# Optimization experiments

Hardware: AMD Instinct MI355X
Metric: run time of the kernel (lower is better)

## Reference

```python
import jax, jax.numpy as jnp
import numpy as np

B, L, H = 1024, 11, 128          # batch, seq_len-1 observations, cde_hidden_dim
VF, IF = 512, 256                # v_f_len, i_f_len
C = H + 1                        # control channels = time + reduced features
SUBSTEPS = 4                     # fixed RK4 substeps per eval interval (stand-in for solver step control)


def setup_inputs() -> dict:
    key = jax.random.key(0)
    ks = jax.random.split(key, 12)
    rn = lambda k, shape, s: jax.random.normal(k, shape, jnp.float32) * s
    F = VF + IF
    inp = {
        'fv': rn(ks[0], (B, L, VF), 1.0),
        'fi': rn(ks[1], (B, L, IF), 1.0),
        # strictly increasing timestamps
        'ts': jnp.cumsum(jax.random.uniform(ks[2], (B, L + 1), jnp.float32) * 0.1 + 0.01, axis=1),
        'w_red': rn(ks[3], (F, H), F ** -0.5), 'b_red': jnp.zeros((H,), jnp.float32),
        'w_init': rn(ks[4], (C, H), C ** -0.5), 'b_init': jnp.zeros((H,), jnp.float32),
        'w_h1': rn(ks[5], (H, H), H ** -0.5), 'b_h1': jnp.zeros((H,), jnp.float32),
        'w_h2': rn(ks[6], (H, H), H ** -0.5), 'b_h2': jnp.zeros((H,), jnp.float32),
        'w_out': rn(ks[7], (H, H * C), H ** -0.5), 'b_out': jnp.zeros((H * C,), jnp.float32),
        'w_r1': rn(ks[8], (H, 128), H ** -0.5), 'b_r1': jnp.zeros((128,), jnp.float32),
        'w_r2': rn(ks[9], (128, 6), 128 ** -0.5), 'b_r2': jnp.zeros((6,), jnp.float32),
    }
    return inp


def reference(fv, fi, ts, w_red, b_red, w_init, b_init, w_h1, b_h1, w_h2, b_h2,
              w_out, b_out, w_r1, b_r1, w_r2, b_r2):
    # fuse ('cat') + reduction_net
    fused = jnp.concatenate([fv, fi], axis=-1) @ w_red + b_red            # [B,L,H]
    tsd = (ts - ts[:, :1])[:, 1:, None]                                   # [B,L,1]
    x = jnp.concatenate([tsd, fused], axis=-1)                            # [B,L,C] control path; knots at t=0..L-1
    z0 = x[:, 0] @ w_init + b_init                                        # initial hidden state, [B,H]

    def field(z):                                                         # CDEFunc: [B,H] -> [B,H,C]
        h1 = jax.nn.relu(z @ w_h1 + b_h1)
        h2 = jax.nn.relu(h1 @ w_h2 + b_h2)
        return jnp.tanh(h2 @ w_out + b_out).reshape(-1, H, C)

    def dXdt(t):                                                          # piecewise-linear interpolation derivative
        idx = jnp.clip(jnp.floor(t).astype(jnp.int32), 0, L - 2)
        return x[:, idx + 1] - x[:, idx]                                  # [B,C]

    def vf(t, z):                                                         # dz/dt = f(z) @ dX/dt
        return jnp.einsum('bhc,bc->bh', field(z), dXdt(t))

    eval_times = jnp.linspace(0.1, 1.0, 10, dtype=jnp.float32)
    hstep = (eval_times[1] - eval_times[0]) / SUBSTEPS

    def rk4(z, t):
        k1 = vf(t, z)
        k2 = vf(t + hstep / 2, z + hstep / 2 * k1)
        k3 = vf(t + hstep / 2, z + hstep / 2 * k2)
        k4 = vf(t + hstep, z + hstep * k3)
        return z + hstep / 6 * (k1 + 2 * k2 + 2 * k3 + k4)

    def interval(z, t0):
        def body(zc, j):
            return rk4(zc, t0 + j * hstep), None
        z2, _ = jax.lax.scan(body, z, jnp.arange(SUBSTEPS, dtype=jnp.float32))
        return z2, z2

    _, zs = jax.lax.scan(interval, z0, eval_times[:-1])                   # [9,B,H]
    h_T = jnp.concatenate([z0[None], zs], axis=0).transpose(1, 0, 2)      # [B,10,H]

    a = h_T @ w_r1 + b_r1
    a = jnp.where(a > 0, a, 0.1 * a)                                      # LeakyReLU(0.1)
    poses = a @ w_r2 + b_r2                                               # [B,10,6]
    return poses, h_T[:, -1, :]
```

## Files before the change

kernel.cpp:

```cpp
#include <hip/hip_runtime.h>
#include <stdint.h>

typedef float   f32x4 __attribute__((ext_vector_type(4)));
typedef float   f32x2 __attribute__((ext_vector_type(2)));
typedef int     i32x4 __attribute__((ext_vector_type(4)));
typedef int     i32x2 __attribute__((ext_vector_type(2)));
typedef __bf16  bf16x8 __attribute__((ext_vector_type(8)));

#define DEV __device__ __forceinline__

DEV uint16_t f2bf(float f){
  uint32_t u = __float_as_uint(f);
  u += 0x7fffu + ((u >> 16) & 1u);
  return (uint16_t)(u >> 16);
}
DEV uint32_t pkbf(float lo, float hi){
  uint32_t r;
  asm("v_cvt_pk_bf16_f32 %0, %1, %2" : "=v"(r) : "v"(lo), "v"(hi));
  return r;
}
DEV uint32_t aoff(uint32_t row, uint32_t q){ return (row << 8) + (q ^ ((row & 7u) << 4)); }

DEV f32x4 MFMA(bf16x8 a, bf16x8 b, f32x4 c){
  return __builtin_amdgcn_mfma_f32_16x16x32_bf16(a, b, c, 0, 0, 0);
}
DEV bf16x8 as_bf(i32x4 v){ union { i32x4 i; bf16x8 b; } u; u.i = v; return u.b; }

DEV uint64_t ld_ic64(const void* p){
  return __hip_atomic_load((const uint64_t*)p, __ATOMIC_RELAXED, __HIP_MEMORY_SCOPE_AGENT);
}
DEV void st_ic64(void* p, uint64_t v){
  __hip_atomic_store((uint64_t*)p, v, __ATOMIC_RELAXED, __HIP_MEMORY_SCOPE_AGENT);
}

__global__ __launch_bounds__(256) void pose_convW(const float* __restrict__ src,
    uint16_t* __restrict__ Wg, uint16_t* __restrict__ w0f)
{
  __shared__ float tile[32][256];
  const float SC = 2.8853900817779268f;
  int bk = blockIdx.x & 3, bn = blockIdx.x >> 2;
  int k0 = bk * 32, n0 = bn * 256;
  int t = threadIdx.x;
  for (int r = 0; r < 32; r++){
    int n = n0 + t;
    tile[r][t] = (n < 16512) ? src[(size_t)(k0 + r) * 16512 + n] : 0.f;
  }
  __syncthreads();
  int n = n0 + t;
  if (n < 16512){
    int c = n % 129, hfull = n / 129;
    int ht = hfull >> 2;
    #pragma unroll
    for (int o = 0; o < 4; o++){
      uint32_t w0 = (uint32_t)f2bf(tile[o*8+0][t]*SC) | ((uint32_t)f2bf(tile[o*8+1][t]*SC) << 16);
      uint32_t w1 = (uint32_t)f2bf(tile[o*8+2][t]*SC) | ((uint32_t)f2bf(tile[o*8+3][t]*SC) << 16);
      uint32_t w2 = (uint32_t)f2bf(tile[o*8+4][t]*SC) | ((uint32_t)f2bf(tile[o*8+5][t]*SC) << 16);
      uint32_t w3 = (uint32_t)f2bf(tile[o*8+6][t]*SC) | ((uint32_t)f2bf(tile[o*8+7][t]*SC) << 16);
      i32x4 val = { (int)w0, (int)w1, (int)w2, (int)w3 };
      uint32_t kg = (uint32_t)(k0 + o*8);
      if (c > 0){
        uint32_t r = (uint32_t)(c - 1)*4 + (hfull & 3);
        uint32_t byte = (uint32_t)ht*131072u + r*256u + ((kg*2u) ^ ((r & 7u) << 4));
        *(i32x4*)((char*)Wg + byte) = val;
      } else {
        uint32_t r0 = (uint32_t)(hfull & 3);
        uint32_t byte = (uint32_t)ht*4096u + (kg >> 5)*1024u + (r0 + 16u*((kg >> 3) & 3u))*16u;
        *(i32x4*)((char*)w0f + byte) = val;
      }
    }
  }
}

__global__ __launch_bounds__(256) void pose_convC(const float* __restrict__ w_h1,
    const float* __restrict__ w_h2, uint32_t* __restrict__ w1f, uint32_t* __restrict__ w2f)
{
  const float* src = blockIdx.x ? w_h2 : w_h1;
  uint32_t* dst = blockIdx.x ? w2f : w1f;
  int t = threadIdx.x;
  for (int ii = 0; ii < 32; ii++){
    int u = t*32 + ii;
    int p = u & 3, l = (u >> 2) & 63, kb = (u >> 8) & 3, Mt = u >> 10;
    int k = kb*32 + (l >> 4)*8 + 2*p;
    int n = Mt*16 + (l & 15);
    uint32_t v = (uint32_t)f2bf(src[(size_t)k*128 + n]) |
                 ((uint32_t)f2bf(src[(size_t)(k+1)*128 + n]) << 16);
    dst[u] = v;
  }
}

__global__ __launch_bounds__(256) void pose_misc(const float* __restrict__ b_out,
    const float* __restrict__ ts, float* __restrict__ bo_f, float* __restrict__ bo_t,
    float* __restrict__ d0t)
{
  const float SC = 2.8853900817779268f;
  int i = blockIdx.x * 256 + threadIdx.x;
  if (i < 16512){
    int c = i % 129, h = i / 129;
    if (c == 0) bo_t[h] = b_out[i] * SC;
    else        bo_f[(size_t)(c-1)*128 + h] = b_out[i] * SC;
  }
  if (i < 1024) d0t[i] = ts[i*12 + 2] - ts[i*12 + 1];
}

__global__ __launch_bounds__(256) void pose_fused(
    const float* __restrict__ fv, const float* __restrict__ fi,
    const float* __restrict__ w_red, const float* __restrict__ b_red,
    float* __restrict__ F0, float* __restrict__ d0f)
{
  __shared__ float pk[128][16];
  __shared__ float res[16][128];
  const int b0 = blockIdx.x * 8;
  const int t = threadIdx.x;
  const int h = t & 127, sg = t >> 7;
  float acc[8] = {0.f,0.f,0.f,0.f,0.f,0.f,0.f,0.f};
  for (int p = 0; p < 6; p++){
    __syncthreads();
    { const int s  = t >> 4;
      const int ch = (t & 15) * 8;
      const int b  = b0 + (s & 7);
      const int ll = s >> 3;
      const int kb = p*128 + ch;
      const float* src = (kb < 512) ? (fv + ((size_t)b*11 + ll)*512 + kb)
                                    : (fi + ((size_t)b*11 + ll)*256 + (kb - 512));
      float v[8];
      #pragma unroll
      for (int j = 0; j < 8; j++) v[j] = src[j];
      #pragma unroll
      for (int j = 0; j < 8; j++) pk[ch + j][s] = v[j];
    }
    __syncthreads();
    #pragma unroll 4
    for (int kk = 0; kk < 128; kk++){
      const float wv = w_red[(size_t)(p*128 + kk)*128 + h];
      f32x4 v0 = *(const f32x4*)&pk[kk][sg*8];
      f32x4 v1 = *(const f32x4*)&pk[kk][sg*8 + 4];
      acc[0] += v0.x*wv; acc[1] += v0.y*wv; acc[2] += v0.z*wv; acc[3] += v0.w*wv;
      acc[4] += v1.x*wv; acc[5] += v1.y*wv; acc[6] += v1.z*wv; acc[7] += v1.w*wv;
    }
  }
  __syncthreads();
  const float br = b_red[h];
  #pragma unroll
  for (int si = 0; si < 8; si++) res[sg*8 + si][h] = acc[si] + br;
  __syncthreads();
  if (sg == 0){
    #pragma unroll
    for (int si = 0; si < 8; si++){
      const int b = b0 + si;
      const float f0 = res[si][h];
      const float f1 = res[8 + si][h];
      F0[(size_t)b*128 + h] = f0;
      d0f[(size_t)h*1024 + b] = f1 - f0;
    }
  }
}

DEV uint32_t zaddr(int b, int h){
  return (uint32_t)(b >> 7)*32768u + (uint32_t)((b >> 4) & 7)*4096u + (uint32_t)(h >> 5)*1024u
       + ((uint32_t)(b & 15) + 16u*(((uint32_t)h & 31u) >> 3))*16u + ((uint32_t)h & 7u)*2u;
}

__global__ __launch_bounds__(512) void pose_init(
    const float* __restrict__ F0, const float* __restrict__ ts,
    const float* __restrict__ w_init, const float* __restrict__ b_init,
    const float* __restrict__ d0f, const float* __restrict__ d0t,
    float* __restrict__ z_base, uint16_t* __restrict__ zfG,
    float* __restrict__ hT, float* __restrict__ S)
{
  __shared__ float Ft[128][64];
  const int b0 = blockIdx.x * 64;
  const int t = threadIdx.x;
  { const int b = t >> 3, ch = (t & 7)*16;
    #pragma unroll
    for (int j = 0; j < 16; j++) Ft[ch + j][b] = F0[(size_t)(b0 + b)*128 + ch + j];
  }
  __syncthreads();
  const int h = t & 127, rg = t >> 7;
  float acc[16];
  const float w0 = w_init[h], bi = b_init[h];
  #pragma unroll
  for (int r = 0; r < 16; r++){
    const int b = b0 + rg*16 + r;
    acc[r] = (ts[b*12 + 1] - ts[b*12 + 0]) * w0 + bi;
  }
  #pragma unroll 2
  for (int j = 0; j < 128; j++){
    const float wv = w_init[(j + 1)*128 + h];
    const float* pr = &Ft[j][rg*16];
    #pragma unroll
    for (int q = 0; q < 4; q++){
      f32x4 v = *(const f32x4*)(pr + q*4);
      acc[q*4+0] += v.x*wv; acc[q*4+1] += v.y*wv; acc[q*4+2] += v.z*wv; acc[q*4+3] += v.w*wv;
    }
  }
  #pragma unroll
  for (int r = 0; r < 16; r++){
    const int b = b0 + rg*16 + r;
    const float z = acc[r];
    z_base[(size_t)b*128 + h] = z;
    hT[(size_t)b*1280 + h] = z;
    *(uint16_t*)((char*)zfG + zaddr(b, h)) = f2bf(z);
  }
  if (t < 64){
    const int b = b0 + t;
    float s = d0t[b];
    for (int j = 0; j < 128; j++) s += d0f[(size_t)j*1024 + b];
    S[b] = s;
  }
}

__global__ __launch_bounds__(1024, 1)
__attribute__((amdgpu_num_vgpr(128)))
void pose_persist(
    const uint16_t* __restrict__ Wg, const uint32_t* __restrict__ w1f,
    const uint32_t* __restrict__ w2f, const uint16_t* __restrict__ w0f,
    const float* __restrict__ b1, const float* __restrict__ b2,
    const float* __restrict__ bo_f, const float* __restrict__ bo_t,
    const float* __restrict__ d0f, const float* __restrict__ d0t,
    const float* __restrict__ Sv, const float* __restrict__ z_base,
    uint16_t* __restrict__ zfG, float* __restrict__ hT, uint32_t* __restrict__ bar)
{
  __shared__ __align__(16) char Lds[163840];
  const uint32_t HB = 131072u;
  const int t    = threadIdx.x;
  const int blk  = blockIdx.x;
  const int bt   = blk & 7;
  const int ht   = blk >> 3;
  const int w    = t >> 6, l = t & 63;
  const int l15  = l & 15, l4g = l >> 4;
  const int m8   = w & 7;
  const int half = w >> 3;
  const int m4   = w & 3;
  const int nq   = w >> 2;

  { const i32x4* src = (const i32x4*)((const char*)Wg + (size_t)ht*131072);
    i32x4* dst = (i32x4*)Lds;
    #pragma unroll
    for (int i = 0; i < 8; i++) dst[t + 1024*i] = src[t + 1024*i];
  }

  const float* d0q  = d0f + (size_t)l4g*1024 + bt*128 + nq*32 + l15;
  const float* d0tq = d0t + bt*128 + nq*32 + l15;

  const int bl = t >> 2, hp = t & 3;
  const float HS = 0x1.999996p-6f;
  const float C2 = HS * 0.5f, C6 = HS / 6.f;
  float zb = 0.f, Sb = 0.f, av = 0.f;
  if (t < 512){
    zb = z_base[(size_t)(bt*128 + bl)*128 + ht*4 + hp];
    Sb = Sv[bt*128 + bl];
  }
  uint32_t* cnt = bar + bt*32;
  uint32_t* go  = bar + 256 + bt*32;
  const uint32_t zsl_off = (uint32_t)bt*32768u;
  __syncthreads();

  #pragma unroll 1
  for (int e = 0; e < 144; e++){
    { const char* zsrc = (const char*)zfG + (size_t)(e & 1)*262144 + zsl_off;
      #pragma unroll
      for (int i = 0; i < 2; i++){
        union { uint64_t q[2]; i32x4 v; } u;
        u.q[0] = ld_ic64(zsrc + t*16 + i*16384);
        u.q[1] = ld_ic64(zsrc + t*16 + i*16384 + 8);
        *(i32x4*)(Lds + HB + t*16 + i*16384) = u.v;
      }
    }
    __syncthreads();

    uint32_t pv1[4][2];
    { bf16x8 w1A[4];
      #pragma unroll
      for (int kb = 0; kb < 4; kb++)
        w1A[kb] = as_bf(*(const i32x4*)((const char*)w1f + (size_t)(m8*4 + kb)*1024 + l*16));
      const f32x4 b1v = *(const f32x4*)(b1 + m8*16 + l4g*4);
      #pragma unroll
      for (int nt2 = 0; nt2 < 4; nt2++){
        bf16x8 bz[4];
        #pragma unroll
        for (int kb = 0; kb < 4; kb++)
          bz[kb] = as_bf(*(const i32x4*)(Lds + HB + (uint32_t)(half*4 + nt2)*4096u + kb*1024 + l*16));
        f32x4 a = {0.f,0.f,0.f,0.f};
        #pragma unroll
        for (int kb = 0; kb < 4; kb++) a = MFMA(w1A[kb], bz[kb], a);
        pv1[nt2][0] = pkbf(fmaxf(a.x + b1v.x, 0.f), fmaxf(a.y + b1v.y, 0.f));
        pv1[nt2][1] = pkbf(fmaxf(a.z + b1v.z, 0.f), fmaxf(a.w + b1v.w, 0.f));
      }
    }
    __syncthreads();

    #pragma unroll
    for (int nt2 = 0; nt2 < 4; nt2++){
      const int col = half*64 + nt2*16 + l15;
      i32x2 pv = { (int)pv1[nt2][0], (int)pv1[nt2][1] };
      *(i32x2*)(Lds + HB + aoff((uint32_t)col, (uint32_t)(m8*16 + l4g*4)*2)) = pv;
    }
    __syncthreads();

    bf16x8 bh1[4];
    #pragma unroll
    for (int kb = 0; kb < 4; kb++)
      bh1[kb] = as_bf(*(const i32x4*)(Lds + HB + aoff((uint32_t)(m8*16 + l15), kb*64 + l4g*16)));
    __syncthreads();
    #pragma unroll
    for (int i = 0; i < 4; i++){
      const int Mt = half*4 + i;
      bf16x8 a2[4];
      #pragma unroll
      for (int kb = 0; kb < 4; kb++)
        a2[kb] = as_bf(*(const i32x4*)((const char*)w2f + (size_t)(Mt*4 + kb)*1024 + l*16));
      f32x4 acc = {0.f,0.f,0.f,0.f};
      #pragma unroll
      for (int kb = 0; kb < 4; kb++) acc = MFMA(a2[kb], bh1[kb], acc);
      const f32x4 b2v = *(const f32x4*)(b2 + Mt*16 + l4g*4);
      i32x2 pv = { (int)pkbf(fmaxf(acc.x + b2v.x, 0.f), fmaxf(acc.y + b2v.y, 0.f)),
                   (int)pkbf(fmaxf(acc.z + b2v.z, 0.f), fmaxf(acc.w + b2v.w, 0.f)) };
      *(i32x2*)(Lds + HB + aoff((uint32_t)(m8*16 + l15), (uint32_t)(Mt*16 + l4g*4)*2)) = pv;
    }
    __syncthreads();

    bf16x8 bh2[2][4];
    #pragma unroll
    for (int n2 = 0; n2 < 2; n2++)
      #pragma unroll
      for (int kb = 0; kb < 4; kb++)
        bh2[n2][kb] = as_bf(*(const i32x4*)(Lds + HB +
            aoff((uint32_t)(nq*32 + n2*16 + l15), kb*64 + l4g*16)));
    __syncthreads();

    f32x4 oacc[2];
    oacc[0] = (f32x4){0.f,0.f,0.f,0.f};
    oacc[1] = (f32x4){0.f,0.f,0.f,0.f};

    #pragma unroll 2
    for (int i = 0; i < 8; i++){
      const int Mt = m4*8 + i;
      bf16x8 A[4];
      #pragma unroll
      for (int kb = 0; kb < 4; kb++)
        A[kb] = as_bf(*(const i32x4*)(Lds + aoff((uint32_t)(Mt*16 + l15), kb*64 + l4g*16)));
      const f32x4 bo4 = *(const f32x4*)(bo_f + (size_t)(Mt*4 + l4g)*128 + ht*4);
      #pragma unroll
      for (int n2 = 0; n2 < 2; n2++){
        f32x4 acc = {0.f,0.f,0.f,0.f};
        #pragma unroll
        for (int kb = 0; kb < 4; kb++) acc = MFMA(A[kb], bh2[n2][kb], acc);
        f32x4 rr;
        rr.x = __builtin_amdgcn_rcpf(__builtin_amdgcn_exp2f(acc.x + bo4.x) + 1.f);
        rr.y = __builtin_amdgcn_rcpf(__builtin_amdgcn_exp2f(acc.y + bo4.y) + 1.f);
        rr.z = __builtin_amdgcn_rcpf(__builtin_amdgcn_exp2f(acc.z + bo4.z) + 1.f);
        rr.w = __builtin_amdgcn_rcpf(__builtin_amdgcn_exp2f(acc.w + bo4.w) + 1.f);
        oacc[n2] += rr * d0q[((size_t)Mt << 12) + n2*16];
      }
    }
    if (m4 == 0){
      bf16x8 A0[4];
      #pragma unroll
      for (int kb = 0; kb < 4; kb++)
        A0[kb] = as_bf(*(const i32x4*)((const char*)w0f + (size_t)ht*4096 + kb*1024 + l*16));
      const f32x4 bt4 = *(const f32x4*)(bo_t + ht*4);
      #pragma unroll
      for (int n2 = 0; n2 < 2; n2++){
        f32x4 acc = {0.f,0.f,0.f,0.f};
        #pragma unroll
        for (int kb = 0; kb < 4; kb++) acc = MFMA(A0[kb], bh2[n2][kb], acc);
        f32x4 rr;
        rr.x = __builtin_amdgcn_rcpf(__builtin_amdgcn_exp2f(acc.x + bt4.x) + 1.f);
        rr.y = __builtin_amdgcn_rcpf(__builtin_amdgcn_exp2f(acc.y + bt4.y) + 1.f);
        rr.z = __builtin_amdgcn_rcpf(__builtin_amdgcn_exp2f(acc.z + bt4.z) + 1.f);
        rr.w = __builtin_amdgcn_rcpf(__builtin_amdgcn_exp2f(acc.w + bt4.w) + 1.f);
        const float dc = (l4g == 0) ? d0tq[n2*16] : 0.f;
        oacc[n2] += rr * dc;
      }
    }

    #pragma unroll
    for (int n2 = 0; n2 < 2; n2++){
      #pragma unroll
      for (int c = 0; c < 4; c++){
        float v = oacc[n2][c];
        v += __shfl_xor(v, 16, 64);
        v += __shfl_xor(v, 32, 64);
        oacc[n2][c] = v;
      }
    }
    if (l < 16){
      #pragma unroll
      for (int n2 = 0; n2 < 2; n2++){
        const int b = nq*32 + n2*16 + l15;
        *(f32x4*)(Lds + HB + m4*2048 + b*16) = oacc[n2];
      }
    }
    __syncthreads();

    if (t < 512){
      float psum = 0.f;
      #pragma unroll
      for (int m = 0; m < 4; m++)
        psum += *(const float*)(Lds + HB + m*2048 + bl*16 + hp*4);
      const float kk = Sb - 2.f*psum;
      const int st = e & 3;
      float ze;
      if (st == 0){      av = kk;        ze = zb + C2*kk; }
      else if (st == 1){ av += 2.f*kk;   ze = zb + C2*kk; }
      else if (st == 2){ av += 2.f*kk;   ze = zb + HS*kk; }
      else {
        zb += C6*(av + kk); ze = zb;
        if ((e & 15) == 15)
          hT[(size_t)(bt*128 + bl)*1280 + (size_t)((e >> 4) + 1)*128 + ht*4 + hp] = zb;
      }
      if (e < 143){
        const uint32_t a0 = pkbf(ze, __shfl_xor(ze, 1, 64));
        const uint32_t b0 = (uint32_t)__shfl_xor((int)a0, 2, 64);
        if ((t & 3) == 0){
          uint64_t zw = (uint64_t)a0 | ((uint64_t)b0 << 32);
          char* zdst = (char*)zfG + (size_t)((e + 1) & 1)*262144 + zsl_off
                     + (bl >> 4)*4096 + (ht >> 3)*1024
                     + ((bl & 15) + 16*((ht >> 1) & 3))*16 + (ht & 1)*8;
          st_ic64(zdst, zw);
        }
        asm volatile("s_waitcnt vmcnt(0)" ::: "memory");
        if ((t & 63) == 0){
          uint32_t a = __hip_atomic_fetch_add(cnt, 1u, __ATOMIC_RELAXED, __HIP_MEMORY_SCOPE_AGENT);
          if (a == 256u*(uint32_t)(e + 1) - 1u)
            __hip_atomic_store(go, (uint32_t)(e + 1), __ATOMIC_RELAXED, __HIP_MEMORY_SCOPE_AGENT);
        }
      }
    }

    if (e < 143){
      const uint32_t ep = (uint32_t)(e + 1);
      int spins = 0;
      while (__hip_atomic_load(go, __ATOMIC_RELAXED, __HIP_MEMORY_SCOPE_AGENT) < ep){
        __builtin_amdgcn_s_sleep(2);
        if (++spins > (1 << 20)) break;
      }
      asm volatile("" ::: "memory");
    }
  }
}

__global__ __launch_bounds__(256) void pose_readout(
    const float* __restrict__ hT, const float* __restrict__ w_r1, const float* __restrict__ b_r1,
    const float* __restrict__ w_r2, const float* __restrict__ b_r2,
    float* __restrict__ out_poses, float* __restrict__ out_z)
{
  if (blockIdx.x >= 320){
    const int cb = blockIdx.x - 320;
    const int base = cb*2048 + threadIdx.x*4;
    #pragma unroll
    for (int p = 0; p < 2; p++){
      const int i = base + p*1024;
      const int b = i >> 7, h = i & 127;
      *(f32x4*)(out_z + i) = *(const f32x4*)(hT + (size_t)b*1280 + 1152 + h);
    }
    return;
  }
  __shared__ float htl[128][32];
  __shared__ float al[32][128];
  const int r0 = blockIdx.x * 32;
  const int t = threadIdx.x;
  { const int row = t >> 3, ch = (t & 7)*16;
    #pragma unroll
    for (int j = 0; j < 16; j++)
      htl[ch + j][row] = hT[(size_t)(r0 + row)*128 + ch + j];
  }
  __syncthreads();
  const int j = t & 127, rg = t >> 7;
  float a[16];
  const float bj = b_r1[j];
  #pragma unroll
  for (int r = 0; r < 16; r++) a[r] = bj;
  #pragma unroll 2
  for (int kk = 0; kk < 128; kk++){
    const float wv = w_r1[(size_t)kk*128 + j];
    const float* pr = &htl[kk][rg*16];
    #pragma unroll
    for (int q = 0; q < 4; q++){
      f32x4 v = *(const f32x4*)(pr + q*4);
      a[q*4+0] += v.x*wv; a[q*4+1] += v.y*wv; a[q*4+2] += v.z*wv; a[q*4+3] += v.w*wv;
    }
  }
  #pragma unroll
  for (int r = 0; r < 16; r++){
    float v = a[r];
    al[rg*16 + r][j] = (v > 0.f) ? v : 0.1f*v;
  }
  __syncthreads();
  if (t < 192){
    const int row = t / 6, p = t % 6;
    float s = b_r2[p];
    const float* ar = al[row];
    #pragma unroll 4
    for (int jj = 0; jj < 128; jj++) s += ar[jj] * w_r2[jj*6 + p];
    out_poses[(size_t)(r0 + row)*6 + p] = s;
  }
}

extern "C" void kernel_launch(void* const* d_in, const int* in_sizes, int n_in,
                              void* d_out, int out_size, void* d_ws, size_t ws_size,
                              hipStream_t stream)
{
  (void)in_sizes; (void)n_in; (void)out_size; (void)ws_size;
  const float* fv    = (const float*)d_in[0];
  const float* fi    = (const float*)d_in[1];
  const float* ts    = (const float*)d_in[2];
  const float* w_red = (const float*)d_in[3];
  const float* b_red = (const float*)d_in[4];
  const float* w_init= (const float*)d_in[5];
  const float* b_init= (const float*)d_in[6];
  const float* w_h1  = (const float*)d_in[7];
  const float* b_h1  = (const float*)d_in[8];
  const float* w_h2  = (const float*)d_in[9];
  const float* b_h2  = (const float*)d_in[10];
  const float* w_out = (const float*)d_in[11];
  const float* b_out = (const float*)d_in[12];
  const float* w_r1  = (const float*)d_in[13];
  const float* b_r1  = (const float*)d_in[14];
  const float* w_r2  = (const float*)d_in[15];
  const float* b_r2  = (const float*)d_in[16];

  char* p = (char*)d_ws;
  auto take = [&](size_t n){ char* r = p; p += (n + 255) & ~(size_t)255; return r; };
  uint32_t* bar   = (uint32_t*)take(4096);
  uint16_t* Wg    = (uint16_t*)take((size_t)32*131072);
  uint16_t* w0f   = (uint16_t*)take((size_t)32*4096);
  uint32_t* w1f   = (uint32_t*)take(32768);
  uint32_t* w2f   = (uint32_t*)take(32768);
  float* bo_f     = (float*)take((size_t)128*128*4);
  float* bo_t     = (float*)take(128*4);
  float* d0f      = (float*)take((size_t)128*1024*4);
  float* d0t      = (float*)take(1024*4);
  float* Sv       = (float*)take(1024*4);
  float* F0       = (float*)take((size_t)1024*128*4);
  float* z_base   = (float*)take((size_t)1024*128*4);
  uint16_t* zfG   = (uint16_t*)take((size_t)2*262144);
  float* hT       = (float*)take((size_t)1024*10*128*4);

  float* out_poses = (float*)d_out;
  float* out_z     = (float*)d_out + 61440;

  hipMemsetAsync(bar, 0, 4096, stream);
  hipMemsetAsync(w0f, 0, (size_t)32*4096*2, stream);
  pose_convW<<<260, 256, 0, stream>>>(w_out, Wg, w0f);
  pose_convC<<<2,   256, 0, stream>>>(w_h1, w_h2, w1f, w2f);
  pose_misc <<<65,  256, 0, stream>>>(b_out, ts, bo_f, bo_t, d0t);
  pose_fused<<<128, 256, 0, stream>>>(fv, fi, w_red, b_red, F0, d0f);
  pose_init <<<16,  512, 0, stream>>>(F0, ts, w_init, b_init, d0f, d0t, z_base, zfG, hT, Sv);

  pose_persist<<<256, 1024, 0, stream>>>(Wg, w1f, w2f, w0f, b_h1, b_h2, bo_f, bo_t,
                                         d0f, d0t, Sv, z_base, zfG, hT, bar);

  pose_readout<<<384, 256, 0, stream>>>(hT, w_r1, b_r1, w_r2, b_r2, out_poses, out_z);
}
```

Measured before the change: 2.937 ms.

## Load z fragments directly from global in first GEMM and spin on one thread

The first MLP layer now reads each wave's z fragments straight from global memory into registers, no longer staging the whole z slice in LDS. Waves are regrouped so each one covers one column tile and four output row tiles, with the bias and ReLU results written straight to LDS. This removes one staging pass and two block barriers per step. The inter-block barrier wait now spins on thread 0 alone with a shorter sleep, followed by __syncthreads, to cut polling traffic, at the cost of an added block barrier.

New measurement: 3.208 ms. 9.2% more time.

```diff
diff --git a/kernel.cpp b/kernel.cpp
--- a/kernel.cpp
+++ b/kernel.cpp
@@ -228,6 +228,8 @@
   const int ht   = blk >> 3;
   const int w    = t >> 6, l = t & 63;
   const int l15  = l & 15, l4g = l >> 4;
+  const int c8   = w & 7;
+  const int mh   = w >> 3;
   const int m8   = w & 7;
   const int half = w >> 3;
   const int m4   = w & 3;
@@ -257,43 +259,31 @@
 
   #pragma unroll 1
   for (int e = 0; e < 144; e++){
-    { const char* zsrc = (const char*)zfG + (size_t)(e & 1)*262144 + zsl_off;
-      #pragma unroll
-      for (int i = 0; i < 2; i++){
-        union { uint64_t q[2]; i32x4 v; } u;
-        u.q[0] = ld_ic64(zsrc + t*16 + i*16384);
-        u.q[1] = ld_ic64(zsrc + t*16 + i*16384 + 8);
-        *(i32x4*)(Lds + HB + t*16 + i*16384) = u.v;
-      }
-    }
-    __syncthreads();
-
-    uint32_t pv1[4][2];
-    { bf16x8 w1A[4];
-      #pragma unroll
-      for (int kb = 0; kb < 4; kb++)
-        w1A[kb] = as_bf(*(const i32x4*)((const char*)w1f + (size_t)(m8*4 + kb)*1024 + l*16));
-      const f32x4 b1v = *(const f32x4*)(b1 + m8*16 + l4g*4);
-      #pragma unroll
-      for (int nt2 = 0; nt2 < 4; nt2++){
-        bf16x8 bz[4];
+    { const char* zev = (const char*)zfG + (size_t)(e & 1)*262144 + zsl_off + (uint32_t)c8*4096u;
+      bf16x8 bz[4];
+      #pragma unroll
+      for (int kb = 0; kb < 4; kb++){
+        const char* a = zev + kb*1024 + l*16;
+        union { uint64_t q[2]; bf16x8 v; } u;
+        u.q[0] = ld_ic64(a); u.q[1] = ld_ic64(a + 8);
+        bz[kb] = u.v;
+      }
+      const int col = c8*16 + l15;
+      #pragma unroll
+      for (int i = 0; i < 4; i++){
+        const int Mt = mh*4 + i;
+        bf16x8 a1[4];
         #pragma unroll
         for (int kb = 0; kb < 4; kb++)
-          bz[kb] = as_bf(*(const i32x4*)(Lds + HB + (uint32_t)(half*4 + nt2)*4096u + kb*1024 + l*16));
+          a1[kb] = as_bf(*(const i32x4*)((const char*)w1f + (size_t)(Mt*4 + kb)*1024 + l*16));
         f32x4 a = {0.f,0.f,0.f,0.f};
         #pragma unroll
-        for (int kb = 0; kb < 4; kb++) a = MFMA(w1A[kb], bz[kb], a);
-        pv1[nt2][0] = pkbf(fmaxf(a.x + b1v.x, 0.f), fmaxf(a.y + b1v.y, 0.f));
-        pv1[nt2][1] = pkbf(fmaxf(a.z + b1v.z, 0.f), fmaxf(a.w + b1v.w, 0.f));
-      }
-    }
-    __syncthreads();
-
-    #pragma unroll
-    for (int nt2 = 0; nt2 < 4; nt2++){
-      const int col = half*64 + nt2*16 + l15;
-      i32x2 pv = { (int)pv1[nt2][0], (int)pv1[nt2][1] };
-      *(i32x2*)(Lds + HB + aoff((uint32_t)col, (uint32_t)(m8*16 + l4g*4)*2)) = pv;
+        for (int kb = 0; kb < 4; kb++) a = MFMA(a1[kb], bz[kb], a);
+        const f32x4 b1v = *(const f32x4*)(b1 + Mt*16 + l4g*4);
+        i32x2 pv = { (int)pkbf(fmaxf(a.x + b1v.x, 0.f), fmaxf(a.y + b1v.y, 0.f)),
+                     (int)pkbf(fmaxf(a.z + b1v.z, 0.f), fmaxf(a.w + b1v.w, 0.f)) };
+        *(i32x2*)(Lds + HB + aoff((uint32_t)col, (uint32_t)(Mt*16 + l4g*4)*2)) = pv;
+      }
     }
     __syncthreads();
 
@@ -429,13 +419,16 @@
     }
 
     if (e < 143){
-      const uint32_t ep = (uint32_t)(e + 1);
-      int spins = 0;
-      while (__hip_atomic_load(go, __ATOMIC_RELAXED, __HIP_MEMORY_SCOPE_AGENT) < ep){
-        __builtin_amdgcn_s_sleep(2);
-        if (++spins > (1 << 20)) break;
-      }
-      asm volatile("" ::: "memory");
+      if (t == 0){
+        const uint32_t ep = (uint32_t)(e + 1);
+        int spins = 0;
+        while (__hip_atomic_load(go, __ATOMIC_RELAXED, __HIP_MEMORY_SCOPE_AGENT) < ep){
+          __builtin_amdgcn_s_sleep(1);
+          if (++spins > (1 << 20)) break;
+        }
+        asm volatile("" ::: "memory");
+      }
+      __syncthreads();
     }
   }
 }
```
